# Optimization experiments

Measured on AMD Instinct MI355X. Metric: run time of the kernel, lower is better.

Reference implementation:

```python
import jax, jax.numpy as jnp
import numpy as np

# --- low precision float format: exp=5, man=2, subnormals, nearest-even ---
EXP, MAN = 5, 2
BIAS = 2 ** (EXP - 1) - 1          # 15
EMIN = 1 - BIAS                     # -14 (min normal exponent; clamping here gives subnormals)
MAXV = (2.0 - 2.0 ** (-MAN)) * 2.0 ** BIAS


def _q(x):
    """Round x to nearest FP(exp=5, man=2) value (subnormals, clipped at max)."""
    ax = jnp.abs(x)
    e = jnp.floor(jnp.log2(jnp.where(ax > 0, ax, 1.0)))
    e = jnp.maximum(e, EMIN)
    scale = jnp.exp2(e - MAN)
    q = jnp.round(x / scale) * scale   # jnp.round = half-to-even
    q = jnp.clip(q, -MAXV, MAXV)
    return jnp.where(ax > 0, q, x).astype(x.dtype)


# Quantizer: forward quantize, straight-through (quantized) backward
@jax.custom_vjp
def fq(x):
    return _q(x)

def _fq_fwd(x):
    return _q(x), None

def _fq_bwd(_, g):
    return (_q(g),)

fq.defvjp(_fq_fwd, _fq_bwd)


def conv_valid(x, w):
    return jax.lax.conv_general_dilated(
        x, w, window_strides=(1, 1), padding='VALID',
        dimension_numbers=('NCHW', 'OIHW', 'NCHW'))


def qconv(x, w):
    # QConv2d: input_quant, weight_quant, conv, output_quant
    return fq(conv_valid(fq(x), fq(w)))


def qlinear(x, W, b):
    # QLinear: input_quant, weight_quant (weights + bias), matmul, output_quant
    return fq(fq(x) @ fq(W).T + fq(b))


def batchnorm(x, gamma, beta, eps=1e-5):
    # training-mode BatchNorm2d over (N,H,W) per channel
    m = x.mean(axis=(0, 2, 3), keepdims=True)
    v = x.var(axis=(0, 2, 3), keepdims=True)
    return (x - m) * jax.lax.rsqrt(v + eps) * gamma[None, :, None, None] + beta[None, :, None, None]


def maxpool2(x):
    return jax.lax.reduce_window(x, -jnp.inf, jax.lax.max,
                                 (1, 1, 2, 2), (1, 1, 2, 2), 'VALID')


def setup_inputs() -> dict:
    key = jax.random.key(0)
    ks = jax.random.split(key, 12)
    B = 8192
    inp = {
        'x':   jax.random.normal(ks[0], (B, 1, 32, 32), jnp.float32),
        'w1':  jax.random.normal(ks[1], (6, 1, 5, 5), jnp.float32) * 0.2,
        'g1':  jnp.ones((6,), jnp.float32),
        'be1': jnp.zeros((6,), jnp.float32),
        'w2':  jax.random.normal(ks[2], (16, 6, 5, 5), jnp.float32) * 0.1,
        'g2':  jnp.ones((16,), jnp.float32),
        'be2': jnp.zeros((16,), jnp.float32),
        'fw1': jax.random.normal(ks[3], (120, 400), jnp.float32) * 0.05,
        'fb1': jnp.zeros((120,), jnp.float32),
        'fw2': jax.random.normal(ks[4], (84, 120), jnp.float32) * 0.09,
        'fb2': jnp.zeros((84,), jnp.float32),
        'fw3': jax.random.normal(ks[5], (10, 84), jnp.float32) * 0.1,
        'fb3': jnp.zeros((10,), jnp.float32),
    }
    return inp


def reference(x, w1, g1, be1, w2, g2, be2, fw1, fb1, fw2, fb2, fw3, fb3):
    x = fq(x)                                   # act_error_quant
    x = qconv(x, w1)                            # conv1 (no bias)
    x = batchnorm(x, g1, be1)                   # bn1
    x = fq(x)                                   # act_error_quant
    x = maxpool2(jax.nn.relu(x))                # relu + 2x2 maxpool -> [B,6,14,14]
    x = qconv(x, w2)                            # conv2 -> [B,16,10,10]
    x = batchnorm(x, g2, be2)                   # bn2
    x = fq(x)
    x = maxpool2(jax.nn.relu(x))                # -> [B,16,5,5]
    x = x.reshape(x.shape[0], -1)               # [B,400]
    x = jax.nn.relu(qlinear(x, fw1, fb1))       # fc1
    x = jax.nn.relu(qlinear(x, fw2, fb2))       # fc2
    x = qlinear(x, fw3, fb3)                    # fc3 -> [B,10]
    return x
```

## Files before the change

### kernel.cpp

```cpp
#include <hip/hip_runtime.h>
#include <hip/hip_bf16.h>


#define BATCH 8192

__device__ __forceinline__ double fq_d(double x) {
    long long b = __double_as_longlong(x);
    long long ab = b & 0x7fffffffffffffffLL;
    if (ab == 0) return x;
    double q;
    if (ab >= 0x3F10000000000000LL) {
        long long r = b + 0x0001FFFFFFFFFFFFLL + ((b >> 50) & 1LL);
        r &= 0xFFFC000000000000LL;
        q = __longlong_as_double(r);
        q = fmin(fmax(q, -57344.0), 57344.0);
    } else {
        q = rint(x * 65536.0) * 1.52587890625e-05;
    }
    return q;
}

__device__ __forceinline__ unsigned short bfbits(double q) {
    __hip_bfloat16 h = __float2bfloat16((float)q);
    return *(unsigned short*)&h;
}

__global__ void kprep(const float* __restrict__ w1, const float* __restrict__ w2,
                      const float* __restrict__ fb1, const float* __restrict__ fb2,
                      const float* __restrict__ fb3, const float* __restrict__ fw1,
                      const float* __restrict__ fw2, const float* __restrict__ fw3,
                      float* __restrict__ qw1, float* __restrict__ qw2,
                      float* __restrict__ qfb1, float* __restrict__ qfb2,
                      float* __restrict__ qfb3, float* __restrict__ Wt1,
                      float* __restrict__ Wt2, float* __restrict__ Wt3) {
    int i = blockIdx.x * 256 + threadIdx.x;
    if (i < 150) { qw1[i] = (float)fq_d((double)w1[i]); return; }
    i -= 150;
    if (i < 2400) { qw2[i] = (float)fq_d((double)w2[i]); return; }
    i -= 2400;
    if (i < 120) { qfb1[i] = (float)fq_d((double)fb1[i]); return; }
    i -= 120;
    if (i < 84) { qfb2[i] = (float)fq_d((double)fb2[i]); return; }
    i -= 84;
    if (i < 10) { qfb3[i] = (float)fq_d((double)fb3[i]); return; }
    i -= 10;
    if (i < 51200) { int k = i / 128, o = i % 128;
        Wt1[i] = (o < 120) ? (float)fq_d((double)fw1[o * 400 + k]) : 0.0f; return; }
    i -= 51200;
    if (i < 15360) { int k = i / 128, o = i % 128;
        Wt2[i] = (o < 84) ? (float)fq_d((double)fw2[o * 120 + k]) : 0.0f; return; }
    i -= 15360;
    if (i < 1344) { int k = i / 16, o = i % 16;
        Wt3[i] = (o < 10) ? (float)fq_d((double)fw3[o * 84 + k]) : 0.0f; return; }
}
#define PREP_TOTAL (150 + 2400 + 120 + 84 + 10 + 51200 + 15360 + 1344)

__global__ __launch_bounds__(256) void kconv1(const float* __restrict__ x,
        const float* __restrict__ qw, __hip_bfloat16* __restrict__ c1,
        int nimg_total, double* __restrict__ st1) {
    __shared__ float sxf[3 * 1056];
    __shared__ double swd[152];
    __shared__ double sred[6][2];
    int t = threadIdx.x;
    int b0 = blockIdx.x * 3;
    int nimg = nimg_total - b0; if (nimg > 3) nimg = 3;
    for (int i = t; i < nimg * 1024; i += 256) {
        int img = i >> 10, idx = i & 1023;
        sxf[img * 1056 + (idx >> 5) * 33 + (idx & 31)] =
            (float)fq_d((double)x[(size_t)(b0 + img) * 1024 + idx]);
    }
    if (t < 150) swd[t] = (double)qw[t];
    if (t >= 192 && t < 204) ((double*)sred)[t - 192] = 0.0;
    __syncthreads();
    int ntask = nimg * 336;
    for (int task = t; task < ntask; task += 256) {
        int img = task / 336; int rr = task % 336;
        int co = rr / 56; int rem = rr % 56;
        int i0 = (rem >> 2) * 2;
        int j0 = (rem & 3) * 7;
        const float* xb = &sxf[img * 1056];
        const double* wp = &swd[co * 25];
        double a0[7], a1[7];
        #pragma unroll
        for (int j = 0; j < 7; ++j) { a0[j] = 0.0; a1[j] = 0.0; }
        double wr[5], wq[5];
        #pragma unroll
        for (int u = 0; u < 6; ++u) {
            const float* xr = &sxf[img * 1056 + (i0 + u) * 33 + j0];
            double xv[11];
            #pragma unroll
            for (int k = 0; k < 11; ++k) xv[k] = (double)xr[k];
            if (u < 5) {
                #pragma unroll
                for (int tt = 0; tt < 5; ++tt) wr[tt] = wp[u * 5 + tt];
                #pragma unroll
                for (int j = 0; j < 7; ++j)
                    a0[j] = fma(xv[j], wr[0], fma(xv[j+1], wr[1], fma(xv[j+2], wr[2],
                            fma(xv[j+3], wr[3], fma(xv[j+4], wr[4], a0[j])))));
            }
            if (u >= 1) {
                #pragma unroll
                for (int j = 0; j < 7; ++j)
                    a1[j] = fma(xv[j], wq[0], fma(xv[j+1], wq[1], fma(xv[j+2], wq[2],
                            fma(xv[j+3], wq[3], fma(xv[j+4], wq[4], a1[j])))));
            }
            #pragma unroll
            for (int tt = 0; tt < 5; ++tt) wq[tt] = wr[tt];
        }
        size_t base = ((size_t)(b0 + img) * 6 + co) * 784 + (size_t)i0 * 28 + j0;
        double s = 0.0, s2 = 0.0;
        #pragma unroll
        for (int j = 0; j < 7; ++j) {
            double q0 = fq_d(a0[j]), q1 = fq_d(a1[j]);
            ((unsigned short*)c1)[base + j]      = bfbits(q0);
            ((unsigned short*)c1)[base + 28 + j] = bfbits(q1);
            s += q0 + q1; s2 += q0 * q0 + q1 * q1;
        }
        atomicAdd(&sred[co][0], s);
        atomicAdd(&sred[co][1], s2);
    }
    __syncthreads();
    if (t < 12) atomicAdd(&st1[t * 32 + (blockIdx.x & 31)], ((double*)sred)[t]);
}

__global__ void kfinal(const double* __restrict__ st, double* __restrict__ mr,
                       int C, double N) {
    int c = threadIdx.x;
    if (c < C) {
        double s = 0.0, s2 = 0.0;
        for (int b = 0; b < 32; ++b) { s += st[c * 64 + b]; s2 += st[c * 64 + 32 + b]; }
        double m = s / N;
        double v = s2 / N - m * m;
        mr[2 * c] = m;
        mr[2 * c + 1] = 1.0 / sqrt(v + 1e-5);
    }
}

__global__ __launch_bounds__(256) void kpool1(const __hip_bfloat16* __restrict__ c1,
        const double* __restrict__ mr1, const float* __restrict__ g1,
        const float* __restrict__ be1, __hip_bfloat16* __restrict__ p1) {
    int idx = blockIdx.x * 256 + threadIdx.x;
    int pp = idx % 7;  int t1 = idx / 7;
    int ph = t1 % 14;  int t2 = t1 / 14;
    int c  = t2 % 6;   int b  = t2 / 6;
    double m = mr1[2 * c], r = mr1[2 * c + 1];
    double gg = (double)g1[c], bb = (double)be1[c];
    bool useMax = (r * gg) >= 0.0;
    const __hip_bfloat16* src = c1 + (((size_t)b * 6 + c) * 28 + 2 * ph) * 28 + 4 * pp;
    ushort4 u0 = *(const ushort4*)src;
    ushort4 u1 = *(const ushort4*)(src + 28);
    float f0 = __bfloat162float(*(__hip_bfloat16*)&u0.x), f1 = __bfloat162float(*(__hip_bfloat16*)&u0.y);
    float f2 = __bfloat162float(*(__hip_bfloat16*)&u0.z), f3 = __bfloat162float(*(__hip_bfloat16*)&u0.w);
    float f4 = __bfloat162float(*(__hip_bfloat16*)&u1.x), f5 = __bfloat162float(*(__hip_bfloat16*)&u1.y);
    float f6 = __bfloat162float(*(__hip_bfloat16*)&u1.z), f7 = __bfloat162float(*(__hip_bfloat16*)&u1.w);
    float va = useMax ? fmaxf(fmaxf(f0, f1), fmaxf(f4, f5))
                      : fminf(fminf(f0, f1), fminf(f4, f5));
    float vb = useMax ? fmaxf(fmaxf(f2, f3), fmaxf(f6, f7))
                      : fminf(fminf(f2, f3), fminf(f6, f7));
    double qa = fq_d((((double)va - m) * r) * gg + bb);
    double qb = fq_d((((double)vb - m) * r) * gg + bb);
    qa = fmax(qa, 0.0); qb = fmax(qb, 0.0);
    ushort2 pk; pk.x = bfbits(qa); pk.y = bfbits(qb);
    *(ushort2*)&p1[((size_t)b * 6 + c) * 196 + ph * 14 + 2 * pp] = pk;
}

__global__ __launch_bounds__(320) void kconv2(const __hip_bfloat16* __restrict__ p1,
        const float* __restrict__ qw, __hip_bfloat16* __restrict__ c2,
        double* __restrict__ st2) {
    __shared__ float sxf[4704];
    __shared__ float swf[2400];
    __shared__ double sred[16][2];
    int t = threadIdx.x;
    int b0 = blockIdx.x * 4;
    for (int i = t; i < 4704; i += 320) sxf[i] = __bfloat162float(p1[(size_t)b0 * 1176 + i]);
    for (int i = t; i < 2400; i += 320) swf[i] = qw[i];
    if (t < 32) ((double*)sred)[t] = 0.0;
    __syncthreads();
    int img = t / 80, r = t % 80;
    int co = r / 5, i0 = (r % 5) * 2;
    const float* xb = &sxf[img * 1176];
    const float* wb = &swf[co * 150];
    double a0[10], a1[10];
    #pragma unroll
    for (int j = 0; j < 10; ++j) { a0[j] = 0.0; a1[j] = 0.0; }
    double wr[5], wq[5];
    for (int ci = 0; ci < 6; ++ci) {
        #pragma unroll
        for (int u = 0; u < 6; ++u) {
            const float* xr = &xb[ci * 196 + (i0 + u) * 14];
            double xv[14];
            #pragma unroll
            for (int k = 0; k < 14; ++k) xv[k] = (double)xr[k];
            if (u < 5) {
                #pragma unroll
                for (int tt = 0; tt < 5; ++tt) wr[tt] = (double)wb[ci * 25 + u * 5 + tt];
                #pragma unroll
                for (int j = 0; j < 10; ++j)
                    a0[j] = fma(xv[j], wr[0], fma(xv[j+1], wr[1], fma(xv[j+2], wr[2],
                            fma(xv[j+3], wr[3], fma(xv[j+4], wr[4], a0[j])))));
            }
            if (u >= 1) {
                #pragma unroll
                for (int j = 0; j < 10; ++j)
                    a1[j] = fma(xv[j], wq[0], fma(xv[j+1], wq[1], fma(xv[j+2], wq[2],
                            fma(xv[j+3], wq[3], fma(xv[j+4], wq[4], a1[j])))));
            }
            #pragma unroll
            for (int tt = 0; tt < 5; ++tt) wq[tt] = wr[tt];
        }
    }
    size_t base = ((size_t)(b0 + img) * 16 + co) * 100 + (size_t)i0 * 10;
    double s = 0.0, s2 = 0.0;
    #pragma unroll
    for (int j = 0; j < 10; ++j) {
        double q0 = fq_d(a0[j]), q1 = fq_d(a1[j]);
        ((unsigned short*)c2)[base + j]      = bfbits(q0);
        ((unsigned short*)c2)[base + 10 + j] = bfbits(q1);
        s += q0 + q1; s2 += q0 * q0 + q1 * q1;
    }
    atomicAdd(&sred[co][0], s);
    atomicAdd(&sred[co][1], s2);
    __syncthreads();
    if (t < 32) atomicAdd(&st2[t * 32 + (blockIdx.x & 31)], ((double*)sred)[t]);
}

__global__ __launch_bounds__(256) void kfc1(const __hip_bfloat16* __restrict__ c2,
        const double* __restrict__ mr2, const float* __restrict__ g2,
        const float* __restrict__ be2, const float* __restrict__ Wt,
        const float* __restrict__ qb, __hip_bfloat16* __restrict__ outb) {
    constexpr int IN = 400, OUT = 120, OUTP = 128, ROWS = 8, BT = 16;
    __shared__ double sx[BT][IN];
    __shared__ double sbn[16][4];
    int t = threadIdx.x;
    int b0 = blockIdx.x * BT;
    if (t < 16) {
        sbn[t][0] = mr2[2 * t]; sbn[t][1] = mr2[2 * t + 1];
        sbn[t][2] = (double)g2[t]; sbn[t][3] = (double)be2[t];
    }
    __syncthreads();
    for (int i = t; i < BT * IN; i += 256) {
        int r = i / IN, k = i % IN;
        int c = k / 25, rem = k % 25;
        int ph = rem / 5, pw = rem % 5;
        const __hip_bfloat16* src = c2 + (((size_t)(b0 + r) * 16 + c) * 10 + 2 * ph) * 10 + 2 * pw;
        double m = sbn[c][0], rr = sbn[c][1], gg = sbn[c][2], bb = sbn[c][3];
        float f0 = __bfloat162float(src[0]),  f1 = __bfloat162float(src[1]);
        float f2 = __bfloat162float(src[10]), f3 = __bfloat162float(src[11]);
        bool useMax = (rr * gg) >= 0.0;
        float v = useMax ? fmaxf(fmaxf(f0, f1), fmaxf(f2, f3))
                         : fminf(fminf(f0, f1), fminf(f2, f3));
        double q = fq_d((((double)v - m) * rr) * gg + bb);
        sx[r][k] = fmax(q, 0.0);
    }
    __syncthreads();
    int o = t % OUTP;
    int g = t / OUTP;
    double acc[ROWS];
    double bias = (o < OUT) ? (double)qb[o] : 0.0;
    #pragma unroll
    for (int r = 0; r < ROWS; ++r) acc[r] = bias;
    #pragma unroll 4
    for (int k = 0; k < IN; ++k) {
        double w = (double)Wt[k * OUTP + o];
        #pragma unroll
        for (int r = 0; r < ROWS; ++r)
            acc[r] = fma(sx[g * ROWS + r][k], w, acc[r]);
    }
    if (o < OUT) {
        #pragma unroll
        for (int r = 0; r < ROWS; ++r) {
            double q = fq_d(acc[r]);
            if (q < 0.0) q = 0.0;
            outb[(size_t)(b0 + g * ROWS + r) * OUT + o] = __float2bfloat16((float)q);
        }
    }
}

template<int IN, int OUT, int OUTP, int ROWS>
__global__ __launch_bounds__(256) void kfc(const __hip_bfloat16* __restrict__ X,
        const float* __restrict__ Wt, const float* __restrict__ qb,
        __hip_bfloat16* __restrict__ outb, float* __restrict__ outf, int do_relu) {
    constexpr int GROUPS = 256 / OUTP;
    constexpr int BT = ROWS * GROUPS;
    __shared__ double sx[BT][IN];
    int t = threadIdx.x;
    int b0 = blockIdx.x * BT;
    for (int i = t; i < BT * IN; i += 256) {
        int r = i / IN, k = i % IN;
        sx[r][k] = (double)__bfloat162float(X[(size_t)(b0 + r) * IN + k]);
    }
    __syncthreads();
    int o = t % OUTP;
    int g = t / OUTP;
    double acc[ROWS];
    double bias = (o < OUT) ? (double)qb[o] : 0.0;
    #pragma unroll
    for (int r = 0; r < ROWS; ++r) acc[r] = bias;
    #pragma unroll 4
    for (int k = 0; k < IN; ++k) {
        double w = (double)Wt[k * OUTP + o];
        #pragma unroll
        for (int r = 0; r < ROWS; ++r)
            acc[r] = fma(sx[g * ROWS + r][k], w, acc[r]);
    }
    if (o < OUT) {
        #pragma unroll
        for (int r = 0; r < ROWS; ++r) {
            double q = fq_d(acc[r]);
            if (do_relu && q < 0.0) q = 0.0;
            size_t b = (size_t)(b0 + g * ROWS + r);
            if (outf) outf[b * OUT + o] = (float)q;
            else      outb[b * OUT + o] = __float2bfloat16((float)q);
        }
    }
}

extern "C" void kernel_launch(void* const* d_in, const int* in_sizes, int n_in,
                              void* d_out, int out_size, void* d_ws, size_t ws_size,
                              hipStream_t stream) {
    const float* x   = (const float*)d_in[0];
    const float* w1  = (const float*)d_in[1];
    const float* g1  = (const float*)d_in[2];
    const float* be1 = (const float*)d_in[3];
    const float* w2  = (const float*)d_in[4];
    const float* g2  = (const float*)d_in[5];
    const float* be2 = (const float*)d_in[6];
    const float* fw1 = (const float*)d_in[7];
    const float* fb1 = (const float*)d_in[8];
    const float* fw2 = (const float*)d_in[9];
    const float* fb2 = (const float*)d_in[10];
    const float* fw3 = (const float*)d_in[11];
    const float* fb3 = (const float*)d_in[12];

    char* ws = (char*)d_ws;
    double* stats1 = (double*)(ws + 0);
    double* stats2 = (double*)(ws + 3072);
    double* mr1    = (double*)(ws + 11264);
    double* mr2    = (double*)(ws + 11392);
    float* qw1  = (float*)(ws + 12288);
    float* qw2  = (float*)(ws + 13312);
    float* qfb1 = (float*)(ws + 23040);
    float* qfb2 = (float*)(ws + 23552);
    float* qfb3 = (float*)(ws + 24064);
    float* Wt1  = (float*)(ws + 24576);
    float* Wt2  = (float*)(ws + 229376);
    float* Wt3  = (float*)(ws + 290816);
    __hip_bfloat16* c1 = (__hip_bfloat16*)(ws + 303104);
    __hip_bfloat16* p1 = (__hip_bfloat16*)(ws + 77373440);
    __hip_bfloat16* c2 = (__hip_bfloat16*)(ws + 303104);
    __hip_bfloat16* a1 = (__hip_bfloat16*)(ws + 303104 + 26214400);
    __hip_bfloat16* a2 = (__hip_bfloat16*)(ws + 303104 + 28180480);

    hipMemsetAsync(ws, 0, 11264, stream);

    kprep<<<(PREP_TOTAL + 255) / 256, 256, 0, stream>>>(
        w1, w2, fb1, fb2, fb3, fw1, fw2, fw3,
        qw1, qw2, qfb1, qfb2, qfb3, Wt1, Wt2, Wt3);

    kconv1<<<(BATCH + 2) / 3, 256, 0, stream>>>(x, qw1, c1, BATCH, stats1);
    kfinal<<<1, 32, 0, stream>>>(stats1, mr1, 6, (double)BATCH * 784.0);
    kpool1<<<BATCH * 6 * 14 * 7 / 256, 256, 0, stream>>>(c1, mr1, g1, be1, p1);
    kconv2<<<BATCH / 4, 320, 0, stream>>>(p1, qw2, c2, stats2);
    kfinal<<<1, 32, 0, stream>>>(stats2, mr2, 16, (double)BATCH * 100.0);
    kfc1<<<BATCH / 16, 256, 0, stream>>>(c2, mr2, g2, be2, Wt1, qfb1, a1);
    kfc<120, 84, 128, 8><<<BATCH / 16, 256, 0, stream>>>(a1, Wt2, qfb2, a2, (float*)nullptr, 1);
    kfc<84, 10, 16, 1><<<BATCH / 16, 256, 0, stream>>>(a2, Wt3, qfb3, (__hip_bfloat16*)nullptr, (float*)d_out, 0);
}
```

Measured before the change: 436.4 us.

## Split conv work to one output row per thread and fuse fc2/fc3 kernels

Conv1 and conv2 now have each thread compute a single output row instead of two rows that shared input loads, with fewer images per block and more blocks. Conv2 stores results as packed pairs. The fc2 and fc3 layers are merged into one kernel that keeps the fc2 activations in shared memory, removing an intermediate global buffer and a launch. The trade-off is lost input-row reuse in the conv kernels in exchange for more parallelism and fewer registers.

```diff
diff --git a/kernel.cpp b/kernel.cpp
--- a/kernel.cpp
+++ b/kernel.cpp
@@ -57,14 +57,13 @@
 
 __global__ __launch_bounds__(256) void kconv1(const float* __restrict__ x,
         const float* __restrict__ qw, __hip_bfloat16* __restrict__ c1,
-        int nimg_total, double* __restrict__ st1) {
-    __shared__ float sxf[3 * 1056];
+        double* __restrict__ st1) {
+    __shared__ float sxf[2 * 1056];
     __shared__ double swd[152];
     __shared__ double sred[6][2];
     int t = threadIdx.x;
-    int b0 = blockIdx.x * 3;
-    int nimg = nimg_total - b0; if (nimg > 3) nimg = 3;
-    for (int i = t; i < nimg * 1024; i += 256) {
+    int b0 = blockIdx.x * 2;
+    for (int i = t; i < 2048; i += 256) {
         int img = i >> 10, idx = i & 1023;
         sxf[img * 1056 + (idx >> 5) * 33 + (idx & 31)] =
             (float)fq_d((double)x[(size_t)(b0 + img) * 1024 + idx]);
@@ -72,49 +71,35 @@
     if (t < 150) swd[t] = (double)qw[t];
     if (t >= 192 && t < 204) ((double*)sred)[t - 192] = 0.0;
     __syncthreads();
-    int ntask = nimg * 336;
-    for (int task = t; task < ntask; task += 256) {
-        int img = task / 336; int rr = task % 336;
-        int co = rr / 56; int rem = rr % 56;
-        int i0 = (rem >> 2) * 2;
+    for (int task = t; task < 1344; task += 256) {
+        int img = task / 672; int rr = task % 672;
+        int co = rr / 112; int rem = rr % 112;
+        int i0 = rem >> 2;
         int j0 = (rem & 3) * 7;
         const float* xb = &sxf[img * 1056];
         const double* wp = &swd[co * 25];
-        double a0[7], a1[7];
-        #pragma unroll
-        for (int j = 0; j < 7; ++j) { a0[j] = 0.0; a1[j] = 0.0; }
-        double wr[5], wq[5];
-        #pragma unroll
-        for (int u = 0; u < 6; ++u) {
-            const float* xr = &sxf[img * 1056 + (i0 + u) * 33 + j0];
+        double acc[7];
+        #pragma unroll
+        for (int j = 0; j < 7; ++j) acc[j] = 0.0;
+        #pragma unroll
+        for (int u = 0; u < 5; ++u) {
+            const float* xr = &xb[(i0 + u) * 33 + j0];
             double xv[11];
             #pragma unroll
             for (int k = 0; k < 11; ++k) xv[k] = (double)xr[k];
-            if (u < 5) {
-                #pragma unroll
-                for (int tt = 0; tt < 5; ++tt) wr[tt] = wp[u * 5 + tt];
-                #pragma unroll
-                for (int j = 0; j < 7; ++j)
-                    a0[j] = fma(xv[j], wr[0], fma(xv[j+1], wr[1], fma(xv[j+2], wr[2],
-                            fma(xv[j+3], wr[3], fma(xv[j+4], wr[4], a0[j])))));
-            }
-            if (u >= 1) {
-                #pragma unroll
-                for (int j = 0; j < 7; ++j)
-                    a1[j] = fma(xv[j], wq[0], fma(xv[j+1], wq[1], fma(xv[j+2], wq[2],
-                            fma(xv[j+3], wq[3], fma(xv[j+4], wq[4], a1[j])))));
-            }
-            #pragma unroll
-            for (int tt = 0; tt < 5; ++tt) wq[tt] = wr[tt];
+            double w0 = wp[u*5], w1 = wp[u*5+1], w2 = wp[u*5+2], w3 = wp[u*5+3], w4 = wp[u*5+4];
+            #pragma unroll
+            for (int j = 0; j < 7; ++j)
+                acc[j] = fma(xv[j], w0, fma(xv[j+1], w1, fma(xv[j+2], w2,
+                         fma(xv[j+3], w3, fma(xv[j+4], w4, acc[j])))));
         }
         size_t base = ((size_t)(b0 + img) * 6 + co) * 784 + (size_t)i0 * 28 + j0;
         double s = 0.0, s2 = 0.0;
         #pragma unroll
         for (int j = 0; j < 7; ++j) {
-            double q0 = fq_d(a0[j]), q1 = fq_d(a1[j]);
-            ((unsigned short*)c1)[base + j]      = bfbits(q0);
-            ((unsigned short*)c1)[base + 28 + j] = bfbits(q1);
-            s += q0 + q1; s2 += q0 * q0 + q1 * q1;
+            double q = fq_d(acc[j]);
+            ((unsigned short*)c1)[base + j] = bfbits(q);
+            s += q; s2 += q * q;
         }
         atomicAdd(&sred[co][0], s);
         atomicAdd(&sred[co][1], s2);
@@ -167,55 +152,45 @@
 __global__ __launch_bounds__(320) void kconv2(const __hip_bfloat16* __restrict__ p1,
         const float* __restrict__ qw, __hip_bfloat16* __restrict__ c2,
         double* __restrict__ st2) {
-    __shared__ float sxf[4704];
+    __shared__ float sxf[2352];
     __shared__ float swf[2400];
     __shared__ double sred[16][2];
     int t = threadIdx.x;
-    int b0 = blockIdx.x * 4;
-    for (int i = t; i < 4704; i += 320) sxf[i] = __bfloat162float(p1[(size_t)b0 * 1176 + i]);
+    int b0 = blockIdx.x * 2;
+    for (int i = t; i < 2352; i += 320) sxf[i] = __bfloat162float(p1[(size_t)b0 * 1176 + i]);
     for (int i = t; i < 2400; i += 320) swf[i] = qw[i];
     if (t < 32) ((double*)sred)[t] = 0.0;
     __syncthreads();
-    int img = t / 80, r = t % 80;
-    int co = r / 5, i0 = (r % 5) * 2;
+    int img = t / 160, r = t % 160;
+    int co = r / 10, i0 = r % 10;
     const float* xb = &sxf[img * 1176];
     const float* wb = &swf[co * 150];
-    double a0[10], a1[10];
+    double acc[10];
     #pragma unroll
-    for (int j = 0; j < 10; ++j) { a0[j] = 0.0; a1[j] = 0.0; }
-    double wr[5], wq[5];
+    for (int j = 0; j < 10; ++j) acc[j] = 0.0;
     for (int ci = 0; ci < 6; ++ci) {
         #pragma unroll
-        for (int u = 0; u < 6; ++u) {
+        for (int u = 0; u < 5; ++u) {
             const float* xr = &xb[ci * 196 + (i0 + u) * 14];
             double xv[14];
             #pragma unroll
             for (int k = 0; k < 14; ++k) xv[k] = (double)xr[k];
-            if (u < 5) {
-                #pragma unroll
-                for (int tt = 0; tt < 5; ++tt) wr[tt] = (double)wb[ci * 25 + u * 5 + tt];
-                #pragma unroll
-                for (int j = 0; j < 10; ++j)
-                    a0[j] = fma(xv[j], wr[0], fma(xv[j+1], wr[1], fma(xv[j+2], wr[2],
-                            fma(xv[j+3], wr[3], fma(xv[j+4], wr[4], a0[j])))));
-            }
-            if (u >= 1) {
-                #pragma unroll
-                for (int j = 0; j < 10; ++j)
-                    a1[j] = fma(xv[j], wq[0], fma(xv[j+1], wq[1], fma(xv[j+2], wq[2],
-                            fma(xv[j+3], wq[3], fma(xv[j+4], wq[4], a1[j])))));
-            }
-            #pragma unroll
-            for (int tt = 0; tt < 5; ++tt) wq[tt] = wr[tt];
+            double w0 = (double)wb[ci*25+u*5],   w1 = (double)wb[ci*25+u*5+1];
+            double w2 = (double)wb[ci*25+u*5+2], w3 = (double)wb[ci*25+u*5+3];
+            double w4 = (double)wb[ci*25+u*5+4];
+            #pragma unroll
+            for (int j = 0; j < 10; ++j)
+                acc[j] = fma(xv[j], w0, fma(xv[j+1], w1, fma(xv[j+2], w2,
+                         fma(xv[j+3], w3, fma(xv[j+4], w4, acc[j])))));
         }
     }
     size_t base = ((size_t)(b0 + img) * 16 + co) * 100 + (size_t)i0 * 10;
     double s = 0.0, s2 = 0.0;
     #pragma unroll
-    for (int j = 0; j < 10; ++j) {
-        double q0 = fq_d(a0[j]), q1 = fq_d(a1[j]);
-        ((unsigned short*)c2)[base + j]      = bfbits(q0);
-        ((unsigned short*)c2)[base + 10 + j] = bfbits(q1);
+    for (int j = 0; j < 10; j += 2) {
+        double q0 = fq_d(acc[j]), q1 = fq_d(acc[j+1]);
+        ushort2 pk; pk.x = bfbits(q0); pk.y = bfbits(q1);
+        *(ushort2*)((unsigned short*)c2 + base + j) = pk;
         s += q0 + q1; s2 += q0 * q0 + q1 * q1;
     }
     atomicAdd(&sred[co][0], s);
@@ -276,42 +251,49 @@
     }
 }
 
-template<int IN, int OUT, int OUTP, int ROWS>
-__global__ __launch_bounds__(256) void kfc(const __hip_bfloat16* __restrict__ X,
-        const float* __restrict__ Wt, const float* __restrict__ qb,
-        __hip_bfloat16* __restrict__ outb, float* __restrict__ outf, int do_relu) {
-    constexpr int GROUPS = 256 / OUTP;
-    constexpr int BT = ROWS * GROUPS;
-    __shared__ double sx[BT][IN];
+__global__ __launch_bounds__(256) void kfc23(const __hip_bfloat16* __restrict__ a1,
+        const float* __restrict__ Wt2, const float* __restrict__ qfb2,
+        const float* __restrict__ Wt3, const float* __restrict__ qfb3,
+        float* __restrict__ out) {
+    __shared__ double sx1[16][120];
+    __shared__ double s2[16][84];
     int t = threadIdx.x;
-    int b0 = blockIdx.x * BT;
-    for (int i = t; i < BT * IN; i += 256) {
-        int r = i / IN, k = i % IN;
-        sx[r][k] = (double)__bfloat162float(X[(size_t)(b0 + r) * IN + k]);
-    }
-    __syncthreads();
-    int o = t % OUTP;
-    int g = t / OUTP;
-    double acc[ROWS];
-    double bias = (o < OUT) ? (double)qb[o] : 0.0;
-    #pragma unroll
-    for (int r = 0; r < ROWS; ++r) acc[r] = bias;
-    #pragma unroll 4
-    for (int k = 0; k < IN; ++k) {
-        double w = (double)Wt[k * OUTP + o];
-        #pragma unroll
-        for (int r = 0; r < ROWS; ++r)
-            acc[r] = fma(sx[g * ROWS + r][k], w, acc[r]);
-    }
-    if (o < OUT) {
-        #pragma unroll
-        for (int r = 0; r < ROWS; ++r) {
-            double q = fq_d(acc[r]);
-            if (do_relu && q < 0.0) q = 0.0;
-            size_t b = (size_t)(b0 + g * ROWS + r);
-            if (outf) outf[b * OUT + o] = (float)q;
-            else      outb[b * OUT + o] = __float2bfloat16((float)q);
-        }
+    int b0 = blockIdx.x * 16;
+    for (int i = t; i < 16 * 120; i += 256) {
+        int r = i / 120, k = i % 120;
+        sx1[r][k] = (double)__bfloat162float(a1[(size_t)(b0 + r) * 120 + k]);
+    }
+    __syncthreads();
+    {
+        int o = t % 128, g = t / 128;
+        double acc[8];
+        double bias = (o < 84) ? (double)qfb2[o] : 0.0;
+        #pragma unroll
+        for (int r = 0; r < 8; ++r) acc[r] = bias;
+        #pragma unroll 4
+        for (int k = 0; k < 120; ++k) {
+            double w = (double)Wt2[k * 128 + o];
+            #pragma unroll
+            for (int r = 0; r < 8; ++r)
+                acc[r] = fma(sx1[g * 8 + r][k], w, acc[r]);
+        }
+        if (o < 84) {
+            #pragma unroll
+            for (int r = 0; r < 8; ++r) {
+                double q = fq_d(acc[r]);
+                s2[g * 8 + r][o] = fmax(q, 0.0);
+            }
+        }
+    }
+    __syncthreads();
+    {
+        int o = t % 16, g = t / 16;
+        double acc = (o < 10) ? (double)qfb3[o] : 0.0;
+        #pragma unroll 4
+        for (int k = 0; k < 84; ++k)
+            acc = fma(s2[g][k], (double)Wt3[k * 16 + o], acc);
+        if (o < 10)
+            out[(size_t)(b0 + g) * 10 + o] = (float)fq_d(acc);
     }
 }
 
@@ -349,7 +331,6 @@
     __hip_bfloat16* p1 = (__hip_bfloat16*)(ws + 77373440);
     __hip_bfloat16* c2 = (__hip_bfloat16*)(ws + 303104);
     __hip_bfloat16* a1 = (__hip_bfloat16*)(ws + 303104 + 26214400);
-    __hip_bfloat16* a2 = (__hip_bfloat16*)(ws + 303104 + 28180480);
 
     hipMemsetAsync(ws, 0, 11264, stream);
 
@@ -357,12 +338,11 @@
         w1, w2, fb1, fb2, fb3, fw1, fw2, fw3,
         qw1, qw2, qfb1, qfb2, qfb3, Wt1, Wt2, Wt3);
 
-    kconv1<<<(BATCH + 2) / 3, 256, 0, stream>>>(x, qw1, c1, BATCH, stats1);
+    kconv1<<<BATCH / 2, 256, 0, stream>>>(x, qw1, c1, stats1);
     kfinal<<<1, 32, 0, stream>>>(stats1, mr1, 6, (double)BATCH * 784.0);
     kpool1<<<BATCH * 6 * 14 * 7 / 256, 256, 0, stream>>>(c1, mr1, g1, be1, p1);
-    kconv2<<<BATCH / 4, 320, 0, stream>>>(p1, qw2, c2, stats2);
+    kconv2<<<BATCH / 2, 320, 0, stream>>>(p1, qw2, c2, stats2);
     kfinal<<<1, 32, 0, stream>>>(stats2, mr2, 16, (double)BATCH * 100.0);
     kfc1<<<BATCH / 16, 256, 0, stream>>>(c2, mr2, g2, be2, Wt1, qfb1, a1);
-    kfc<120, 84, 128, 8><<<BATCH / 16, 256, 0, stream>>>(a1, Wt2, qfb2, a2, (float*)nullptr, 1);
-    kfc<84, 10, 16, 1><<<BATCH / 16, 256, 0, stream>>>(a2, Wt3, qfb3, (__hip_bfloat16*)nullptr, (float*)d_out, 0);
-}
+    kfc23<<<BATCH / 16, 256, 0, stream>>>(a1, Wt2, qfb2, Wt3, qfb3, (float*)d_out);
+}
```

Result: slower. 462.0 us (+5.9%).
